# Optimization experiments

Hardware: AMD Instinct MI355X
Metric: run time of the kernel (lower is better)

Reference implementation:

```python
import jax, jax.numpy as jnp
import numpy as np

B, S, A, C, E, H = 256, 512, 8, 256, 64, 256

def _lin_params(key, din, dout):
    k1, k2 = jax.random.split(key)
    bound = 1.0 / np.sqrt(din)
    w = jax.random.uniform(k1, (din, dout), minval=-bound, maxval=bound, dtype=jnp.float32)
    b = jax.random.uniform(k2, (dout,), minval=-bound, maxval=bound, dtype=jnp.float32)
    return w, b

def setup_inputs() -> dict:
    key = jax.random.key(0)
    ks = jax.random.split(key, 9)
    q = jax.random.normal(ks[0], (B, S, A), dtype=jnp.float32)
    st = jax.random.normal(ks[1], (B, S, C), dtype=jnp.float32)
    w1a, b1a = _lin_params(ks[2], C, H)
    w1b, b1b = _lin_params(ks[3], H, A * E)
    w2a, b2a = _lin_params(ks[4], C, H)
    w2b, b2b = _lin_params(ks[5], H, E)
    wb1, bb1 = _lin_params(ks[6], C, E)
    wb2a, bb2a = _lin_params(ks[7], C, H)
    wb2b, bb2b = _lin_params(ks[8], H, 1)
    return dict(agent_q_values=q, central_states=st,
                w1a=w1a, b1a=b1a, w1b=w1b, b1b=b1b,
                w2a=w2a, b2a=b2a, w2b=w2b, b2b=b2b,
                wb1=wb1, bb1=bb1,
                wb2a=wb2a, bb2a=bb2a, wb2b=wb2b, bb2b=bb2b)

def _mlp(x, wa, ba, wb, bb):
    # Linear -> ELU -> Linear
    h = jax.nn.elu(x @ wa + ba)
    return h @ wb + bb

def reference(agent_q_values, central_states,
              w1a, b1a, w1b, b1b,
              w2a, b2a, w2b, b2b,
              wb1, bb1,
              wb2a, bb2a, wb2b, bb2b):
    bsz, seq, na = agent_q_values.shape
    st = central_states.reshape(-1, C)                      # [N, C]
    q = agent_q_values.reshape(-1, na)                      # [N, A]
    w1 = jnp.abs(_mlp(st, w1a, b1a, w1b, b1b)).reshape(-1, na, E)   # [N, A, E]
    b1 = st @ wb1 + bb1                                     # [N, E]
    w2 = jnp.abs(_mlp(st, w2a, b2a, w2b, b2b))              # [N, E]
    b2 = _mlp(st, wb2a, bb2a, wb2b, bb2b)                   # [N, 1]
    hidden = jax.nn.relu(jnp.einsum('na,nae->ne', q, w1) + b1)      # [N, E]
    joint = jnp.einsum('ne,ne->n', hidden, w2)[:, None] + b2        # [N, 1]
    return joint.reshape(bsz, seq, 1)
```

## Files before the change

### kernel.cpp

```cpp
#include <hip/hip_runtime.h>
#include <math.h>

typedef __bf16 bf16_t;
typedef bf16_t bf16x8 __attribute__((ext_vector_type(8)));
typedef float  floatx4 __attribute__((ext_vector_type(4)));

#define MFMA16(a, b, c) __builtin_amdgcn_mfma_f32_16x16x32_bf16((a), (b), (c), 0, 0, 0)

constexpr int NTOT = 256 * 512;
constexpr int CDIM = 256;

constexpr int N_TILES  = 88;
constexpr int WS_ELEMS = N_TILES * 4096;

__global__ void prep_weights(const float* __restrict__ w1a, const float* __restrict__ w1b,
                             const float* __restrict__ w2a, const float* __restrict__ w2b,
                             const float* __restrict__ wb1, const float* __restrict__ wb2a,
                             bf16_t* __restrict__ ws) {
  int idx = blockIdx.x * 256 + threadIdx.x;
  if (idx >= WS_ELEMS) return;
  int t   = idx >> 12;
  int rel = idx & 4095;
  const float* src; int dout; int ct;
  if      (t < 16) { src = w1a;  dout = 256; ct = t; }
  else if (t < 20) { src = wb1;  dout = 64;  ct = t - 16; }
  else if (t < 52) { src = w1b;  dout = 512; ct = t - 20; }
  else if (t < 68) { src = w2a;  dout = 256; ct = t - 52; }
  else if (t < 72) { src = w2b;  dout = 64;  ct = t - 68; }
  else             { src = wb2a; dout = 256; ct = t - 72; }
  int j    = rel & 7;
  int lane = (rel >> 3) & 63;
  int ks   = rel >> 9;
  int o = ct * 16 + (lane & 15);
  int k = ks * 32 + (lane >> 4) * 8 + j;
  ws[idx] = (bf16_t)src[(size_t)k * dout + o];
}

__device__ __forceinline__ void gload_lds16(const bf16_t* g, bf16_t* l) {
  __builtin_amdgcn_global_load_lds(
      (const __attribute__((address_space(1))) unsigned int*)g,
      (__attribute__((address_space(3))) unsigned int*)l, 16, 0, 0);
}

__global__ __launch_bounds__(512, 2)
void mixing_fused(const float* __restrict__ q,
                  const float* __restrict__ st,
                  const bf16_t* __restrict__ W,
                  const float* __restrict__ b1a, const float* __restrict__ b1b,
                  const float* __restrict__ b2a, const float* __restrict__ b2b,
                  const float* __restrict__ bb1,
                  const float* __restrict__ bb2a,
                  const float* __restrict__ wb2b, const float* __restrict__ bb2b,
                  float* __restrict__ out) {
  __shared__ __align__(16) bf16_t wbuf[2][8192];
  __shared__ __align__(16) bf16_t t_s[8][32][36];
  __shared__ __align__(16) float  q_s[8][256];

  const int tid  = threadIdx.x;
  const int wid  = tid >> 6;
  const int lane = tid & 63;
  const int l15  = lane & 15;
  const int quad = lane >> 4;
  const int m0   = blockIdx.x * 256 + wid * 32;

  auto stage = [&](int g) {
    const bf16_t* src = W + (size_t)g * 8192 + wid * 1024 + lane * 8;
    bf16_t* dst = &wbuf[g & 1][wid * 1024];
#pragma unroll
    for (int i = 0; i < 2; ++i)
      gload_lds16(src + i * 512, dst + i * 512);
  };

  *(float4*)&q_s[wid][lane * 4] = *(const float4*)(q + (size_t)m0 * 8 + lane * 4);

  bf16x8 sA[2][8];
#pragma unroll
  for (int rt = 0; rt < 2; ++rt) {
    const float* rp = st + (size_t)(m0 + rt * 16 + l15) * CDIM;
#pragma unroll
    for (int ks = 0; ks < 8; ++ks) {
      int k0 = ks * 32 + quad * 8;
      float4 f0 = *(const float4*)(rp + k0);
      float4 f1 = *(const float4*)(rp + k0 + 4);
      bf16x8 v;
      v[0] = (bf16_t)f0.x; v[1] = (bf16_t)f0.y; v[2] = (bf16_t)f0.z; v[3] = (bf16_t)f0.w;
      v[4] = (bf16_t)f1.x; v[5] = (bf16_t)f1.y; v[6] = (bf16_t)f1.z; v[7] = (bf16_t)f1.w;
      sA[rt][ks] = v;
    }
  }

  auto gemmL = [&](int buf, int h, const bf16x8 (&A)[2][8], floatx4 (&acc)[2]) {
    floatx4 z = {0.f, 0.f, 0.f, 0.f};
    acc[0] = z; acc[1] = z;
#pragma unroll
    for (int kk = 0; kk < 8; ++kk) {
      bf16x8 b = *(const bf16x8*)&wbuf[buf][h * 4096 + kk * 512 + lane * 8];
      acc[0] = MFMA16(A[0][kk], b, acc[0]);
      acc[1] = MFMA16(A[1][kk], b, acc[1]);
    }
  };

  stage(0);

  bf16x8 hA[2][8];

#pragma unroll
  for (int ks = 0; ks < 8; ++ks) {
    __syncthreads();
    stage(ks + 1);
    const int buf = ks & 1;
#pragma unroll
    for (int h = 0; h < 2; ++h) {
      int ct = 2 * ks + h;
      floatx4 acc[2];
      gemmL(buf, h, sA, acc);
      float bias = b1a[ct * 16 + l15];
#pragma unroll
      for (int rt = 0; rt < 2; ++rt)
#pragma unroll
        for (int i = 0; i < 4; ++i) {
          float v = acc[rt][i] + bias;
          v = v > 0.f ? v : (__expf(v) - 1.f);
          t_s[wid][rt * 16 + quad * 4 + i][h * 16 + l15] = (bf16_t)v;
        }
    }
#pragma unroll
    for (int rt = 0; rt < 2; ++rt)
      hA[rt][ks] = *(const bf16x8*)&t_s[wid][rt * 16 + l15][quad * 8];
  }

  floatx4 hid[2][4];
#pragma unroll
  for (int gg = 0; gg < 2; ++gg) {
    __syncthreads();
    stage(9 + gg);
    const int buf = gg & 1;
#pragma unroll
    for (int h = 0; h < 2; ++h) {
      int et = 2 * gg + h;
      floatx4 acc[2];
      gemmL(buf, h, sA, acc);
      float bias = bb1[et * 16 + l15];
      hid[0][et] = acc[0] + bias;
      hid[1][et] = acc[1] + bias;
    }
  }

#pragma unroll 1
  for (int a = 0; a < 8; ++a) {
#pragma unroll
    for (int g2 = 0; g2 < 2; ++g2) {
      const int idx = a * 2 + g2;
      __syncthreads();
      stage(11 + idx);
      const int buf = g2;
#pragma unroll
      for (int h = 0; h < 2; ++h) {
        int ct = a * 4 + g2 * 2 + h;
        const int et = g2 * 2 + h;
        floatx4 acc[2];
        gemmL(buf, h, hA, acc);
        float bias = b1b[ct * 16 + l15];
#pragma unroll
        for (int rt = 0; rt < 2; ++rt)
#pragma unroll
          for (int i = 0; i < 4; ++i) {
            float w1v = fabsf(acc[rt][i] + bias);
            float qv  = q_s[wid][(rt * 16 + quad * 4 + i) * 8 + a];
            hid[rt][et][i] += qv * w1v;
          }
      }
    }
  }
#pragma unroll
  for (int rt = 0; rt < 2; ++rt)
#pragma unroll
    for (int et = 0; et < 4; ++et)
#pragma unroll
      for (int i = 0; i < 4; ++i) hid[rt][et][i] = fmaxf(hid[rt][et][i], 0.f);

#pragma unroll
  for (int ks = 0; ks < 8; ++ks) {
    __syncthreads();
    stage(27 + ks);
    const int buf = ks & 1;
#pragma unroll
    for (int h = 0; h < 2; ++h) {
      int ct = 2 * ks + h;
      floatx4 acc[2];
      gemmL(buf, h, sA, acc);
      float bias = b2a[ct * 16 + l15];
#pragma unroll
      for (int rt = 0; rt < 2; ++rt)
#pragma unroll
        for (int i = 0; i < 4; ++i) {
          float v = acc[rt][i] + bias;
          v = v > 0.f ? v : (__expf(v) - 1.f);
          t_s[wid][rt * 16 + quad * 4 + i][h * 16 + l15] = (bf16_t)v;
        }
    }
#pragma unroll
    for (int rt = 0; rt < 2; ++rt)
      hA[rt][ks] = *(const bf16x8*)&t_s[wid][rt * 16 + l15][quad * 8];
  }

  float pj[2][4] = {{0.f, 0.f, 0.f, 0.f}, {0.f, 0.f, 0.f, 0.f}};
#pragma unroll
  for (int gg = 0; gg < 2; ++gg) {
    __syncthreads();
    stage(35 + gg);
    const int buf = gg & 1;
#pragma unroll
    for (int h = 0; h < 2; ++h) {
      int et = 2 * gg + h;
      floatx4 acc[2];
      gemmL(buf, h, hA, acc);
      float bias = b2b[et * 16 + l15];
#pragma unroll
      for (int rt = 0; rt < 2; ++rt)
#pragma unroll
        for (int i = 0; i < 4; ++i) {
          float w2v = fabsf(acc[rt][i] + bias);
          pj[rt][i] += hid[rt][et][i] * w2v;
        }
    }
  }

  float pb[2][4] = {{0.f, 0.f, 0.f, 0.f}, {0.f, 0.f, 0.f, 0.f}};
#pragma unroll 1
  for (int gg = 0; gg < 8; ++gg) {
    __syncthreads();
    if (gg < 7) stage(37 + gg);
    const int buf = gg & 1;
#pragma unroll
    for (int h = 0; h < 2; ++h) {
      int ct = 2 * gg + h;
      floatx4 acc[2];
      gemmL(buf, h, sA, acc);
      float bias = bb2a[ct * 16 + l15];
      float wv   = wb2b[ct * 16 + l15];
#pragma unroll
      for (int rt = 0; rt < 2; ++rt)
#pragma unroll
        for (int i = 0; i < 4; ++i) {
          float v = acc[rt][i] + bias;
          v = v > 0.f ? v : (__expf(v) - 1.f);
          pb[rt][i] += v * wv;
        }
    }
  }

  float bb2 = bb2b[0];
#pragma unroll
  for (int rt = 0; rt < 2; ++rt)
#pragma unroll
    for (int i = 0; i < 4; ++i) {
      float v = pj[rt][i] + pb[rt][i];
      v += __shfl_xor(v, 1);
      v += __shfl_xor(v, 2);
      v += __shfl_xor(v, 4);
      v += __shfl_xor(v, 8);
      if (l15 == 0) out[m0 + rt * 16 + quad * 4 + i] = v + bb2;
    }
}

extern "C" void kernel_launch(void* const* d_in, const int* in_sizes, int n_in,
                              void* d_out, int out_size, void* d_ws, size_t ws_size,
                              hipStream_t stream) {
  const float* q    = (const float*)d_in[0];
  const float* st   = (const float*)d_in[1];
  const float* w1a  = (const float*)d_in[2];
  const float* b1a  = (const float*)d_in[3];
  const float* w1b  = (const float*)d_in[4];
  const float* b1b  = (const float*)d_in[5];
  const float* w2a  = (const float*)d_in[6];
  const float* b2a  = (const float*)d_in[7];
  const float* w2b  = (const float*)d_in[8];
  const float* b2b  = (const float*)d_in[9];
  const float* wb1  = (const float*)d_in[10];
  const float* bb1  = (const float*)d_in[11];
  const float* wb2a = (const float*)d_in[12];
  const float* bb2a = (const float*)d_in[13];
  const float* wb2b = (const float*)d_in[14];
  const float* bb2b = (const float*)d_in[15];
  bf16_t* W = (bf16_t*)d_ws;

  hipLaunchKernelGGL(prep_weights, dim3((WS_ELEMS + 255) / 256), dim3(256), 0, stream,
                     w1a, w1b, w2a, w2b, wb1, wb2a, W);
  hipLaunchKernelGGL(mixing_fused, dim3(NTOT / 256), dim3(512), 0, stream,
                     q, st, W, b1a, b1b, b2a, b2b, bb1, bb2a, wb2b, bb2b, (float*)d_out);
}
```

Measured before the change: 338.1 us.

## Load weight fragments directly from global memory instead of LDS staging

Removes the double-buffered global-to-LDS weight staging and its per-stage block barriers. Each wave now reads its B fragments straight from the pre-swizzled bf16 weight buffer, relying on L1/L2 caching. Blocks shrink from 512 to 256 threads, covering 128 rows each, with twice as many blocks. This trades the barrier stalls and shared-memory traffic for more global/cache load traffic and more register pressure from holding eight B fragments at once.

```diff
diff --git a/kernel.cpp b/kernel.cpp
--- a/kernel.cpp
+++ b/kernel.cpp
@@ -36,13 +36,7 @@
   ws[idx] = (bf16_t)src[(size_t)k * dout + o];
 }
 
-__device__ __forceinline__ void gload_lds16(const bf16_t* g, bf16_t* l) {
-  __builtin_amdgcn_global_load_lds(
-      (const __attribute__((address_space(1))) unsigned int*)g,
-      (__attribute__((address_space(3))) unsigned int*)l, 16, 0, 0);
-}
-
-__global__ __launch_bounds__(512, 2)
+__global__ __launch_bounds__(256, 2)
 void mixing_fused(const float* __restrict__ q,
                   const float* __restrict__ st,
                   const bf16_t* __restrict__ W,
@@ -52,24 +46,15 @@
                   const float* __restrict__ bb2a,
                   const float* __restrict__ wb2b, const float* __restrict__ bb2b,
                   float* __restrict__ out) {
-  __shared__ __align__(16) bf16_t wbuf[2][8192];
-  __shared__ __align__(16) bf16_t t_s[8][32][36];
-  __shared__ __align__(16) float  q_s[8][256];
+  __shared__ __align__(16) bf16_t t_s[4][32][36];
+  __shared__ __align__(16) float  q_s[4][256];
 
   const int tid  = threadIdx.x;
   const int wid  = tid >> 6;
   const int lane = tid & 63;
   const int l15  = lane & 15;
   const int quad = lane >> 4;
-  const int m0   = blockIdx.x * 256 + wid * 32;
-
-  auto stage = [&](int g) {
-    const bf16_t* src = W + (size_t)g * 8192 + wid * 1024 + lane * 8;
-    bf16_t* dst = &wbuf[g & 1][wid * 1024];
-#pragma unroll
-    for (int i = 0; i < 2; ++i)
-      gload_lds16(src + i * 512, dst + i * 512);
-  };
+  const int m0   = blockIdx.x * 128 + wid * 32;
 
   *(float4*)&q_s[wid][lane * 4] = *(const float4*)(q + (size_t)m0 * 8 + lane * 4);
 
@@ -89,31 +74,30 @@
     }
   }
 
-  auto gemmL = [&](int buf, int h, const bf16x8 (&A)[2][8], floatx4 (&acc)[2]) {
+  auto gemmG = [&](int g, int h, const bf16x8 (&A)[2][8], floatx4 (&acc)[2]) {
+    const bf16_t* wp = W + (size_t)g * 8192 + h * 4096 + lane * 8;
+    bf16x8 b[8];
+#pragma unroll
+    for (int kk = 0; kk < 8; ++kk)
+      b[kk] = *(const bf16x8*)(wp + kk * 512);
     floatx4 z = {0.f, 0.f, 0.f, 0.f};
     acc[0] = z; acc[1] = z;
 #pragma unroll
     for (int kk = 0; kk < 8; ++kk) {
-      bf16x8 b = *(const bf16x8*)&wbuf[buf][h * 4096 + kk * 512 + lane * 8];
-      acc[0] = MFMA16(A[0][kk], b, acc[0]);
-      acc[1] = MFMA16(A[1][kk], b, acc[1]);
+      acc[0] = MFMA16(A[0][kk], b[kk], acc[0]);
+      acc[1] = MFMA16(A[1][kk], b[kk], acc[1]);
     }
   };
 
-  stage(0);
-
   bf16x8 hA[2][8];
 
 #pragma unroll
   for (int ks = 0; ks < 8; ++ks) {
-    __syncthreads();
-    stage(ks + 1);
-    const int buf = ks & 1;
 #pragma unroll
     for (int h = 0; h < 2; ++h) {
       int ct = 2 * ks + h;
       floatx4 acc[2];
-      gemmL(buf, h, sA, acc);
+      gemmG(ks, h, sA, acc);
       float bias = b1a[ct * 16 + l15];
 #pragma unroll
       for (int rt = 0; rt < 2; ++rt)
@@ -132,14 +116,11 @@
   floatx4 hid[2][4];
 #pragma unroll
   for (int gg = 0; gg < 2; ++gg) {
-    __syncthreads();
-    stage(9 + gg);
-    const int buf = gg & 1;
 #pragma unroll
     for (int h = 0; h < 2; ++h) {
       int et = 2 * gg + h;
       floatx4 acc[2];
-      gemmL(buf, h, sA, acc);
+      gemmG(8 + gg, h, sA, acc);
       float bias = bb1[et * 16 + l15];
       hid[0][et] = acc[0] + bias;
       hid[1][et] = acc[1] + bias;
@@ -151,15 +132,12 @@
 #pragma unroll
     for (int g2 = 0; g2 < 2; ++g2) {
       const int idx = a * 2 + g2;
-      __syncthreads();
-      stage(11 + idx);
-      const int buf = g2;
 #pragma unroll
       for (int h = 0; h < 2; ++h) {
         int ct = a * 4 + g2 * 2 + h;
         const int et = g2 * 2 + h;
         floatx4 acc[2];
-        gemmL(buf, h, hA, acc);
+        gemmG(10 + idx, h, hA, acc);
         float bias = b1b[ct * 16 + l15];
 #pragma unroll
         for (int rt = 0; rt < 2; ++rt)
@@ -181,14 +159,11 @@
 
 #pragma unroll
   for (int ks = 0; ks < 8; ++ks) {
-    __syncthreads();
-    stage(27 + ks);
-    const int buf = ks & 1;
 #pragma unroll
     for (int h = 0; h < 2; ++h) {
       int ct = 2 * ks + h;
       floatx4 acc[2];
-      gemmL(buf, h, sA, acc);
+      gemmG(26 + ks, h, sA, acc);
       float bias = b2a[ct * 16 + l15];
 #pragma unroll
       for (int rt = 0; rt < 2; ++rt)
@@ -207,14 +182,11 @@
   float pj[2][4] = {{0.f, 0.f, 0.f, 0.f}, {0.f, 0.f, 0.f, 0.f}};
 #pragma unroll
   for (int gg = 0; gg < 2; ++gg) {
-    __syncthreads();
-    stage(35 + gg);
-    const int buf = gg & 1;
 #pragma unroll
     for (int h = 0; h < 2; ++h) {
       int et = 2 * gg + h;
       floatx4 acc[2];
-      gemmL(buf, h, hA, acc);
+      gemmG(34 + gg, h, hA, acc);
       float bias = b2b[et * 16 + l15];
 #pragma unroll
       for (int rt = 0; rt < 2; ++rt)
@@ -229,14 +201,11 @@
   float pb[2][4] = {{0.f, 0.f, 0.f, 0.f}, {0.f, 0.f, 0.f, 0.f}};
 #pragma unroll 1
   for (int gg = 0; gg < 8; ++gg) {
-    __syncthreads();
-    if (gg < 7) stage(37 + gg);
-    const int buf = gg & 1;
 #pragma unroll
     for (int h = 0; h < 2; ++h) {
       int ct = 2 * gg + h;
       floatx4 acc[2];
-      gemmL(buf, h, sA, acc);
+      gemmG(36 + gg, h, sA, acc);
       float bias = bb2a[ct * 16 + l15];
       float wv   = wb2b[ct * 16 + l15];
 #pragma unroll
@@ -287,6 +256,6 @@
 
   hipLaunchKernelGGL(prep_weights, dim3((WS_ELEMS + 255) / 256), dim3(256), 0, stream,
                      w1a, w1b, w2a, w2b, wb1, wb2a, W);
-  hipLaunchKernelGGL(mixing_fused, dim3(NTOT / 256), dim3(512), 0, stream,
+  hipLaunchKernelGGL(mixing_fused, dim3(NTOT / 128), dim3(256), 0, stream,
                      q, st, W, b1a, b1b, b2a, b2b, bb1, bb2a, wb2b, bb2b, (float*)d_out);
 }
```

Measured after the change: 366.4 us. +8.3%, slower.
